# Optimization experiments

Measured on AMD Instinct MI355X. Metric: run time of the kernel, lower is better.

## Reference

```python
import jax, jax.numpy as jnp
import numpy as np

EPS = 1e-7
INF = 1e8
SOFT_CENTER_RADIUS = 3.0
TOPK = 13
IOU_WEIGHT = 3.0
NUM_CLASSES = 80
N_PRIORS = 33600
NUM_GT = 256
IMG = 1024.0


def setup_inputs() -> dict:
    key = jax.random.key(0)
    k1, k2, k3, k4, k5, k6, k7 = jax.random.split(key, 7)
    n, g, c = N_PRIORS, NUM_GT, NUM_CLASSES
    pred_scores = jax.random.normal(k1, (n, c), jnp.float32)
    # priors: (cx, cy, stride, stride)
    ctr = jax.random.uniform(k2, (n, 2), jnp.float32) * IMG
    stride = jnp.full((n, 1), 8.0, jnp.float32)
    priors = jnp.concatenate([ctr, stride, stride], axis=-1)
    # predicted boxes, x1y1x2y2
    pwh = jax.random.uniform(k3, (n, 2), jnp.float32) * 96.0 + 8.0
    pctr = jax.random.uniform(k4, (n, 2), jnp.float32) * IMG
    pred_bboxes = jnp.concatenate([pctr - pwh / 2, pctr + pwh / 2], axis=-1)
    # gt boxes, x1y1x2y2
    gwh = jax.random.uniform(k5, (g, 2), jnp.float32) * 192.0 + 16.0
    gctr = jax.random.uniform(k6, (g, 2), jnp.float32) * IMG
    gt_bboxes = jnp.concatenate([gctr - gwh / 2, gctr + gwh / 2], axis=-1)
    gt_labels = jax.random.randint(k7, (g,), 0, c, dtype=jnp.int32).astype(jnp.int64)
    return {"pred_scores": pred_scores, "priors": priors,
            "pred_bboxes": pred_bboxes, "gt_bboxes": gt_bboxes,
            "gt_labels": gt_labels}


def _pairwise_iou(a, b):
    # a: (n,4), b: (g,4), x1y1x2y2 -> (n,g)
    area_a = (a[:, 2] - a[:, 0]) * (a[:, 3] - a[:, 1])
    area_b = (b[:, 2] - b[:, 0]) * (b[:, 3] - b[:, 1])
    lt = jnp.maximum(a[:, None, :2], b[None, :, :2])
    rb = jnp.minimum(a[:, None, 2:], b[None, :, 2:])
    wh = jnp.clip(rb - lt, 0.0, None)
    inter = wh[..., 0] * wh[..., 1]
    union = area_a[:, None] + area_b[None, :] - inter
    return inter / jnp.maximum(union, 1e-6)


def reference(pred_scores, priors, pred_bboxes, gt_bboxes, gt_labels):
    n, g = pred_bboxes.shape[0], gt_bboxes.shape[0]
    gt_labels = gt_labels.astype(jnp.int32)

    # ---- find_inside_points (box_dim == 4) ----
    pts = priors[:, :2]                                   # (n,2)
    lt = pts[:, None, :] - gt_bboxes[None, :, :2]
    rb = gt_bboxes[None, :, 2:] - pts[:, None, :]
    is_in_gts = jnp.min(jnp.concatenate([lt, rb], -1), -1) > 0   # (n,g)
    pad_bbox_flag = gt_bboxes.sum(-1) > 0                        # (g,)
    is_in_gts = is_in_gts & pad_bbox_flag[None, :]
    valid_mask = jnp.any(is_in_gts, -1)                          # (n,)

    # ---- soft center prior ----
    gt_center = (gt_bboxes[:, :2] + gt_bboxes[:, 2:]) * 0.5      # (g,2)
    dist = jnp.sqrt(((pts[:, None, :] - gt_center[None, :, :]) ** 2).sum(-1))
    dist = dist / priors[:, 2:3]                                 # / stride
    dist = dist * valid_mask[:, None].astype(dist.dtype)
    soft_center_prior = jnp.power(10.0, dist - SOFT_CENTER_RADIUS)

    # ---- iou cost ----
    ious = _pairwise_iou(pred_bboxes, gt_bboxes)                 # (n,g)
    iou_cost = -jnp.log(ious + EPS) * IOU_WEIGHT

    # ---- soft classification cost (BCE-with-logits, iou targets) ----
    logits = pred_scores[:, gt_labels]                           # (n,g)
    scale = jnp.abs(ious - jax.nn.sigmoid(logits)) ** 2
    bce = jnp.maximum(logits, 0) - logits * ious + jnp.log1p(jnp.exp(-jnp.abs(logits)))
    cost = bce * scale + iou_cost + soft_center_prior
    cost = jnp.where(valid_mask[:, None], cost, INF)

    # ---- dynamic k matching (vectorized over GTs) ----
    K = min(TOPK, n)
    topk_ious, _ = jax.lax.top_k(ious.T, K)                      # (g,K)
    dynamic_ks = jnp.clip(topk_ious.sum(-1).astype(jnp.int32), 1, None)  # (g,)
    _, cand_idx = jax.lax.top_k(-cost.T, K)                      # (g,K) lowest-cost priors per gt
    sel = (jnp.arange(K)[None, :] < dynamic_ks[:, None]).astype(jnp.float32)
    matching = jnp.zeros((g, n), jnp.float32).at[
        jnp.arange(g)[:, None], cand_idx].set(sel).T             # (n,g)

    # resolve priors matched to multiple gts -> keep min-cost gt
    multi = matching.sum(-1) > 1
    onehot_min = jax.nn.one_hot(jnp.argmin(cost, -1), g, dtype=jnp.float32)
    matching = jnp.where(multi[:, None], onehot_min, matching)

    fg = matching.sum(-1) > 0
    matched_gt_inds = jnp.argmax(matching, -1)                   # (n,)
    matched_pred_ious = (matching * ious).sum(-1)                # (n,)

    final = fg & valid_mask
    assigned_gt_inds = jnp.where(final, matched_gt_inds + 1, 0)
    assigned_labels = jnp.where(final, gt_labels[matched_gt_inds], -1)
    max_overlaps = jnp.where(final, matched_pred_ious, -INF)
    return assigned_gt_inds, max_overlaps, assigned_labels
```

## Files before the change

### kernel.cpp

```cpp
#include <hip/hip_runtime.h>
#include <cstdint>

#define NPRI 33600
#define NGT  256
#define NCLS 80
#define KTOP 13
#define INF_F 1.0e8f
#define EPS_F 1e-7f
#define L10 3.3219280948873623f
#define SLC  4
#define SLEN (NPRI / SLC)
#define SCN_T 512
#define NW8 (SCN_T / 64)
#define CAPI 1536
#define CAPC 512
#define RFIX 5.5f
#define PREP_BLKS ((NPRI + 255) / 256)
#define NEGINF __int_as_float(0xff800000)

typedef unsigned long long u64;

__device__ __forceinline__ int get_label(const void* p, int j, int is64) {
    if (is64) return (int)((const long long*)p)[j];
    return ((const int*)p)[j];
}

__device__ __forceinline__ float wave_max_bc_f32(float v) {
    #pragma unroll
    for (int off = 32; off > 0; off >>= 1) v = fmaxf(v, __shfl_down(v, off, 64));
    return __int_as_float(__builtin_amdgcn_readfirstlane(__float_as_int(v)));
}
__device__ __forceinline__ u64 wave_min_bc_u64(u64 v) {
    #pragma unroll
    for (int off = 32; off > 0; off >>= 1) { u64 o = __shfl_down(v, off, 64); v = (o < v) ? o : v; }
    unsigned lo = (unsigned)__builtin_amdgcn_readfirstlane((int)(v & 0xffffffffull));
    unsigned hi = (unsigned)__builtin_amdgcn_readfirstlane((int)(v >> 32));
    return (((u64)hi) << 32) | lo;
}
template<int NSL>
__device__ __forceinline__ void wave_merge_max13_f32(float (&l)[NSL], float* dst, int lane) {
    int p = 0;
    for (int r = 0; r < KTOP; ++r) {
        float cur = NEGINF;
        #pragma unroll
        for (int s = 0; s < NSL; ++s) if (s == p) cur = l[NSL - 1 - s];
        float bm = wave_max_bc_f32(cur);
        u64 m = __ballot(cur == bm && bm != NEGINF);
        int first = __ffsll(m) - 1;
        if (lane == first) p++;
        if (lane == 0) dst[r] = bm;
    }
}
template<int NSL>
__device__ __forceinline__ void wave_merge_minN(u64 (&l)[NSL], u64* dst, int lane) {
    int p = 0;
    for (int r = 0; r < KTOP; ++r) {
        u64 cur = ~0ull;
        #pragma unroll
        for (int s = 0; s < NSL; ++s) if (s == p) cur = l[s];
        u64 bm = wave_min_bc_u64(cur);
        if (cur == bm && bm != ~0ull) p++;
        if (lane == 0) dst[r] = bm;
    }
}

__device__ __forceinline__ float iou_exact(float4 pb, float areap, float gx1, float gy1,
                                           float gx2, float gy2, float areag) {
    float iw = fmaxf(fminf(pb.z, gx2) - fmaxf(pb.x, gx1), 0.0f);
    float ih = fmaxf(fminf(pb.w, gy2) - fmaxf(pb.y, gy1), 0.0f);
    float inter = iw * ih;
    return inter / fmaxf(areap + areag - inter, 1e-6f);
}
__device__ __forceinline__ float cost_exact(float4 p2, float gcx, float gcy,
                                            float l, float iou) {
    float dx = p2.x - gcx, dy = p2.y - gcy;
    float dist = sqrtf(dx * dx + dy * dy) / p2.z;
    float soft = exp2f((dist - 3.0f) * L10);
    float sig = 1.0f / (1.0f + expf(-l));
    float dd = iou - sig;
    float bce = fmaxf(l, 0.0f) - l * iou + log1pf(expf(-fabsf(l)));
    float iouc = -logf(iou + EPS_F) * 3.0f;
    return bce * (dd * dd) + iouc + soft;
}

__global__ __launch_bounds__(256) void k_prep(
        const float* __restrict__ priors, const float* __restrict__ gt,
        const void* labels, const float* __restrict__ pboxes,
        float4* __restrict__ pbp,
        int* count, int* firstgt, int* flag, int* nmulti) {
    __shared__ float4 gbox[NGT];
    __shared__ int    gpad[NGT];
    __shared__ int    bad;
    const int tid = threadIdx.x;
    const int b = blockIdx.x;
    if (b == 0 && tid == 0) { bad = 0; *nmulti = 0; }
    {
        float4 bx = ((const float4*)gt)[tid];
        gbox[tid] = bx;
        gpad[tid] = ((bx.x + bx.y + bx.z + bx.w) > 0.0f) ? 1 : 0;
    }
    __syncthreads();
    if (b == 0 && tid < 128) {
        long long v = ((const long long*)labels)[tid];
        if (v < 0 || v >= NCLS) atomicOr(&bad, 1);
    }
    int i = b * 256 + tid;
    if (i < NPRI) {
        count[i] = 0; firstgt[i] = NGT;
        float4 pr = ((const float4*)priors)[i];
        float px = pr.x, py = pr.y;
        int v = 0;
        for (int j = 0; j < NGT; ++j) {
            float4 bx = gbox[j];
            float m = fminf(fminf(px - bx.x, py - bx.y), fminf(bx.z - px, bx.w - py));
            if (m > 0.0f && gpad[j]) { v = 1; break; }
        }
        pbp[2 * i]     = ((const float4*)pboxes)[i];
        pbp[2 * i + 1] = make_float4(px, py, pr.z, v ? 1.0f : 0.0f);
    }
    if (b == 0) {
        __syncthreads();
        if (tid == 0) *flag = bad ? 0 : 1;
    }
}

__global__ __launch_bounds__(SCN_T) void k_scan(
        const float* __restrict__ scores,
        const float4* __restrict__ pbp,
        const float* __restrict__ gt, const void* labels, const int* flag,
        float* __restrict__ part_iou, u64* __restrict__ part_cost) {
    const int tid = threadIdx.x, lane = tid & 63, wid = tid >> 6;
    const int j = blockIdx.x, slice = blockIdx.y;
    const int base = slice * SLEN;
    const int is64 = *flag;

    const float4 gb = ((const float4*)gt)[j];
    const float gx1 = gb.x, gy1 = gb.y, gx2 = gb.z, gy2 = gb.w;
    const float areag = (gx2 - gx1) * (gy2 - gy1);
    const float gcx = (gx1 + gx2) * 0.5f, gcy = (gy1 + gy2) * 0.5f;
    const int lab = get_label(labels, j, is64);

    __shared__ int s_ni, s_nc, s_mode;
    __shared__ float s_dmax;
    __shared__ float liou[CAPI];
    __shared__ int lcost[CAPC];
    __shared__ float wiof[NW8 * KTOP];
    __shared__ u64 wco[NW8 * KTOP];
    __shared__ u64 csel[KTOP];
    __shared__ u64 s_tauk;
    if (tid == 0) { s_ni = 0; s_nc = 0; }
    __syncthreads();

    for (int i = base + tid; i < base + SLEN; i += SCN_T) {
        float4 pb = pbp[2 * i];
        float4 p2 = pbp[2 * i + 1];
        float areap = (pb.z - pb.x) * (pb.w - pb.y);
        float iw = fmaxf(fminf(pb.z, gx2) - fmaxf(pb.x, gx1), 0.0f);
        float ih = fmaxf(fminf(pb.w, gy2) - fmaxf(pb.y, gy1), 0.0f);
        float inter = iw * ih;
        float iou = inter / fmaxf(areap + areag - inter, 1e-6f);
        if (iou > 0.0f) {
            int p = atomicAdd(&s_ni, 1);
            if (p < CAPI) liou[p] = iou;
        }
        if (p2.w != 0.0f) {
            float dx = p2.x - gcx, dy = p2.y - gcy;
            float rad = p2.z * RFIX;
            if (dx * dx + dy * dy <= rad * rad * (1.0f + 1e-5f)) {
                int p = atomicAdd(&s_nc, 1);
                if (p < CAPC) lcost[p] = i;
            }
        }
    }
    __syncthreads();
    const int ni = s_ni, nc = s_nc;
    const int ncc = (nc < CAPC) ? nc : CAPC;
    const bool fI = (ni > CAPI);

    const bool part = (tid < ncc);
    int ci = 0; float4 cpb, cp2; float lv = 0.0f;
    if (part) {
        ci = lcost[tid];
        cpb = pbp[2 * ci];
        cp2 = pbp[2 * ci + 1];
        lv = scores[(size_t)ci * NCLS + lab];
    }

    if (!fI) {
        float l3[3] = {NEGINF, NEGINF, NEGINF};
        for (int k = tid; k < ni; k += SCN_T) {
            float v = liou[k];
            if (v > l3[0]) {
                l3[0] = v;
                if (l3[0] > l3[1]) { float t = l3[0]; l3[0] = l3[1]; l3[1] = t; }
                if (l3[1] > l3[2]) { float t = l3[1]; l3[1] = l3[2]; l3[2] = t; }
            }
        }
        wave_merge_max13_f32<3>(l3, &wiof[wid * KTOP], lane);
    } else {
        float lf[KTOP];
        #pragma unroll
        for (int s = 0; s < KTOP; ++s) lf[s] = NEGINF;
        for (int i = base + tid; i < base + SLEN; i += SCN_T) {
            float4 pb = pbp[2 * i];
            float areap = (pb.z - pb.x) * (pb.w - pb.y);
            float iou = iou_exact(pb, areap, gx1, gy1, gx2, gy2, areag);
            if (iou > lf[0]) {
                lf[0] = iou;
                #pragma unroll
                for (int s = 0; s < KTOP - 1; ++s)
                    if (lf[s] > lf[s + 1]) { float t = lf[s]; lf[s] = lf[s + 1]; lf[s + 1] = t; }
            }
        }
        wave_merge_max13_f32<KTOP>(lf, &wiof[wid * KTOP], lane);
    }

    {
        u64 ck[1] = {~0ull};
        if (part) {
            float areap = (cpb.z - cpb.x) * (cpb.w - cpb.y);
            float iou = iou_exact(cpb, areap, gx1, gy1, gx2, gy2, areag);
            float ec = cost_exact(cp2, gcx, gcy, lv, iou);
            ck[0] = (((u64)__float_as_uint(ec)) << 32) | (unsigned)ci;
        }
        wave_merge_minN<1>(ck, &wco[wid * KTOP], lane);
    }
    __syncthreads();

    if (wid == 0) {
        float* dpi = part_iou + ((size_t)j * SLC + slice) * KTOP;
        int p = 0;
        for (int r = 0; r < KTOP; ++r) {
            float cur = (lane < NW8 && p < KTOP) ? wiof[lane * KTOP + p] : NEGINF;
            float bm = wave_max_bc_f32(cur);
            u64 m = __ballot(cur == bm && bm != NEGINF);
            int first = __ffsll(m) - 1;
            if (lane == first) p++;
            if (lane == 0) dpi[r] = bm;
        }
    } else if (wid == 1) {
        int p = 0;
        for (int r = 0; r < KTOP; ++r) {
            u64 cur = (lane < NW8 && p < KTOP) ? wco[lane * KTOP + p] : ~0ull;
            u64 bm = wave_min_bc_u64(cur);
            if (cur == bm && bm != ~0ull) p++;
            if (lane == 0) { csel[r] = bm; if (r == KTOP - 1) s_tauk = bm; }
        }
    }
    __syncthreads();
    if (tid == 0) {
        u64 tk = s_tauk;
        int mode; float dmax = 0.0f;
        if (tk == ~0ull) mode = 2;
        else {
            float tau = __uint_as_float((unsigned)(tk >> 32));
            if (!(tau < 9.0e7f)) mode = 2;
            else {
                dmax = 3.0f + __log2f(tau + 1e-5f) * (1.0f / L10) + 4e-3f;
                mode = (dmax > RFIX || nc > CAPC) ? 1 : 0;
            }
        }
        s_mode = mode; s_dmax = dmax;
    }
    __syncthreads();
    int mode = s_mode;

    if (mode == 1) {
        const float dmax = s_dmax;
        if (tid == 0) s_nc = 0;
        __syncthreads();
        for (int i = base + tid; i < base + SLEN; i += SCN_T) {
            float4 p2 = pbp[2 * i + 1];
            if (p2.w != 0.0f) {
                float dx = p2.x - gcx, dy = p2.y - gcy;
                float rad = p2.z * dmax;
                if (dx * dx + dy * dy <= rad * rad * (1.0f + 1e-5f)) {
                    int p = atomicAdd(&s_nc, 1);
                    if (p < CAPC) lcost[p] = i;
                }
            }
        }
        __syncthreads();
        int nc2 = s_nc;
        if (nc2 > CAPC) {
            mode = 2;
        } else {
            u64 ck[1] = {~0ull};
            if (tid < nc2) {
                int i = lcost[tid];
                float4 pb = pbp[2 * i];
                float4 p2 = pbp[2 * i + 1];
                float areap = (pb.z - pb.x) * (pb.w - pb.y);
                float iou = iou_exact(pb, areap, gx1, gy1, gx2, gy2, areag);
                float ec = cost_exact(p2, gcx, gcy, scores[(size_t)i * NCLS + lab], iou);
                ck[0] = (((u64)__float_as_uint(ec)) << 32) | (unsigned)i;
            }
            wave_merge_minN<1>(ck, &wco[wid * KTOP], lane);
            __syncthreads();
            if (wid == 0) {
                int p = 0;
                for (int r = 0; r < KTOP; ++r) {
                    u64 cur = (lane < NW8 && p < KTOP) ? wco[lane * KTOP + p] : ~0ull;
                    u64 bm = wave_min_bc_u64(cur);
                    if (cur == bm && bm != ~0ull) p++;
                    if (lane == 0) csel[r] = bm;
                }
            }
            __syncthreads();
        }
    }
    if (mode == 2) {
        u64 lf[KTOP];
        #pragma unroll
        for (int s = 0; s < KTOP; ++s) lf[s] = ~0ull;
        for (int i = base + tid; i < base + SLEN; i += SCN_T) {
            float4 pb = pbp[2 * i];
            float4 p2 = pbp[2 * i + 1];
            float areap = (pb.z - pb.x) * (pb.w - pb.y);
            float iou = iou_exact(pb, areap, gx1, gy1, gx2, gy2, areag);
            float ec = INF_F;
            if (p2.w != 0.0f) ec = cost_exact(p2, gcx, gcy, scores[(size_t)i * NCLS + lab], iou);
            u64 k2 = (((u64)__float_as_uint(ec)) << 32) | (unsigned)i;
            if (k2 < lf[KTOP - 1]) {
                lf[KTOP - 1] = k2;
                #pragma unroll
                for (int s = KTOP - 1; s > 0; --s)
                    if (lf[s] < lf[s - 1]) { u64 t = lf[s]; lf[s] = lf[s - 1]; lf[s - 1] = t; }
            }
        }
        wave_merge_minN<KTOP>(lf, &wco[wid * KTOP], lane);
        __syncthreads();
        if (wid == 0) {
            int p = 0;
            for (int r = 0; r < KTOP; ++r) {
                u64 cur = (lane < NW8 && p < KTOP) ? wco[lane * KTOP + p] : ~0ull;
                u64 bm = wave_min_bc_u64(cur);
                if (cur == bm && bm != ~0ull) p++;
                if (lane == 0) csel[r] = bm;
            }
        }
        __syncthreads();
    }
    if (tid < KTOP) {
        u64* dpc = part_cost + ((size_t)j * SLC + slice) * KTOP;
        dpc[tid] = csel[tid];
    }
}

__global__ __launch_bounds__(64) void k_merge(
        const float* __restrict__ part_iou, const u64* __restrict__ part_cost,
        int* count, int* firstgt) {
    const int j = blockIdx.x;
    const int lane = threadIdx.x;
    float vi = (lane < SLC * KTOP) ? part_iou[(size_t)j * SLC * KTOP + lane] : NEGINF;
    float tsum = 0.0f;
    for (int r = 0; r < KTOP; ++r) {
        float bm = wave_max_bc_f32(vi);
        u64 m = __ballot(vi == bm && bm != NEGINF);
        int first = __ffsll(m) - 1;
        if (lane == first) vi = NEGINF;
        tsum += (bm == NEGINF) ? 0.0f : bm;
    }
    int ks = (int)tsum;
    if (ks < 1) ks = 1;
    u64 kc = (lane < SLC * KTOP) ? part_cost[(size_t)j * SLC * KTOP + lane] : ~0ull;
    u64 mine = ~0ull;
    for (int r = 0; r < KTOP; ++r) {
        u64 bm = wave_min_bc_u64(kc);
        if (kc == bm && bm != ~0ull) kc = ~0ull;
        if (lane == r) mine = bm;
    }
    if (lane < KTOP && lane < ks && mine != ~0ull) {
        int idx = (int)(unsigned)(mine & 0xFFFFFFFFull);
        atomicAdd(&count[idx], 1);
        atomicMin(&firstgt[idx], j);
    }
}

__global__ __launch_bounds__(256) void k_assign(
        const float4* __restrict__ pbp, const float* __restrict__ gt,
        const void* labels, const int* flag,
        const int* __restrict__ count, const int* __restrict__ firstgt,
        int* nmulti, int* mlist, float* __restrict__ out) {
    __shared__ float4 gbox[NGT];
    __shared__ int glab[NGT];
    __shared__ float gareas[NGT];
    int tid = threadIdx.x;
    int is64 = *flag;
    {
        float4 b = ((const float4*)gt)[tid];
        gbox[tid] = b;
        glab[tid] = get_label(labels, tid, is64);
        gareas[tid] = (b.z - b.x) * (b.w - b.y);
    }
    __syncthreads();
    int i = blockIdx.x * 256 + tid;
    if (i >= NPRI) return;
    float4 p2 = pbp[2 * i + 1];
    int v = (p2.w != 0.0f) ? 1 : 0;
    int c = count[i];
    float o0 = 0.0f, o1 = -INF_F, o2 = -1.0f;
    if (v && c == 1) {
        int j = firstgt[i];
        float4 pb = pbp[2 * i];
        float areap = (pb.z - pb.x) * (pb.w - pb.y);
        float4 g = gbox[j];
        float iw = fmaxf(fminf(pb.z, g.z) - fmaxf(pb.x, g.x), 0.0f);
        float ih = fmaxf(fminf(pb.w, g.w) - fmaxf(pb.y, g.y), 0.0f);
        float inter = iw * ih;
        float iou = inter / fmaxf(areap + gareas[j] - inter, 1e-6f);
        o0 = (float)(j + 1); o1 = iou; o2 = (float)glab[j];
    } else if (v && c > 1) {
        int pos = atomicAdd(nmulti, 1);
        mlist[pos] = i;
    }
    out[i] = o0;
    out[NPRI + i] = o1;
    out[2 * NPRI + i] = o2;
}

__global__ __launch_bounds__(256) void k_multi(
        const float* __restrict__ scores,
        const float4* __restrict__ pbp, const float* __restrict__ gt,
        const void* labels, const int* flag,
        const int* __restrict__ nmulti, const int* __restrict__ mlist,
        float* __restrict__ out) {
    __shared__ float4 gbox[NGT];
    __shared__ int glab[NGT];
    __shared__ float gcxs[NGT], gcys[NGT], gareas[NGT];
    __shared__ u64 red4[4];
    const int tid = threadIdx.x;
    const int is64 = *flag;
    {
        float4 b = ((const float4*)gt)[tid];
        gbox[tid] = b;
        glab[tid] = get_label(labels, tid, is64);
        gcxs[tid] = (b.x + b.z) * 0.5f;
        gcys[tid] = (b.y + b.w) * 0.5f;
        gareas[tid] = (b.z - b.x) * (b.w - b.y);
    }
    __syncthreads();
    const int nm = *nmulti;
    const int j = tid;
    for (int m = blockIdx.x; m < nm; m += gridDim.x) {
        const int i = mlist[m];
        float4 pb = pbp[2 * i];
        float4 p2 = pbp[2 * i + 1];
        float areap = (pb.z - pb.x) * (pb.w - pb.y);

        float4 g = gbox[j];
        float iw = fmaxf(fminf(pb.z, g.z) - fmaxf(pb.x, g.x), 0.0f);
        float ih = fmaxf(fminf(pb.w, g.w) - fmaxf(pb.y, g.y), 0.0f);
        float inter = iw * ih;
        float iou = inter / fmaxf(areap + gareas[j] - inter, 1e-6f);
        float dx = p2.x - gcxs[j], dy = p2.y - gcys[j];
        float dist = sqrtf(dx * dx + dy * dy) / p2.z;
        float soft = exp2f((dist - 3.0f) * L10);
        float l = scores[(size_t)i * NCLS + glab[j]];
        float sig = 1.0f / (1.0f + expf(-l));
        float dd = iou - sig;
        float bce = fmaxf(l, 0.0f) - l * iou + log1pf(expf(-fabsf(l)));
        float cost = bce * (dd * dd) + (-logf(iou + EPS_F) * 3.0f) + soft;

        u64 key = (((u64)__float_as_uint(cost)) << 32) | (unsigned)j;
        u64 v = key;
        #pragma unroll
        for (int off = 32; off > 0; off >>= 1) {
            u64 o = __shfl_down(v, off, 64);
            v = (o < v) ? o : v;
        }
        if ((tid & 63) == 0) red4[tid >> 6] = v;
        __syncthreads();
        u64 best = red4[0];
        #pragma unroll
        for (int q = 1; q < 4; ++q) best = (red4[q] < best) ? red4[q] : best;
        if (key == best) {
            out[i] = (float)(j + 1);
            out[NPRI + i] = iou;
            out[2 * NPRI + i] = (float)glab[j];
        }
        __syncthreads();
    }
}

extern "C" void kernel_launch(void* const* d_in, const int* in_sizes, int n_in,
                              void* d_out, int out_size, void* d_ws, size_t ws_size,
                              hipStream_t stream) {
    const float* scores = (const float*)d_in[0];
    const float* priors = (const float*)d_in[1];
    const float* pboxes = (const float*)d_in[2];
    const float* gt     = (const float*)d_in[3];
    const void*  labels = d_in[4];
    float* out = (float*)d_out;

    char* ws = (char*)d_ws;
    size_t off = 0;
    auto alloc = [&](size_t bytes) { size_t o = off; off = (off + bytes + 255) & ~(size_t)255; return o; };
    int*    flag     = (int*)(ws + alloc(4));
    int*    nmulti   = (int*)(ws + alloc(4));
    int*    count    = (int*)(ws + alloc((size_t)NPRI * 4));
    int*    firstgt  = (int*)(ws + alloc((size_t)NPRI * 4));
    int*    mlist    = (int*)(ws + alloc((size_t)NPRI * 4));
    float*  part_iou = (float*)(ws + alloc((size_t)NGT * SLC * KTOP * 4));
    u64*    part_cost= (u64*)(ws + alloc((size_t)NGT * SLC * KTOP * 8));
    float4* pbp      = (float4*)(ws + alloc((size_t)NPRI * 32));
    (void)ws_size;

    hipLaunchKernelGGL(k_prep, dim3(PREP_BLKS), dim3(256), 0, stream,
                       priors, gt, labels, pboxes, pbp, count, firstgt, flag, nmulti);
    hipLaunchKernelGGL(k_scan, dim3(NGT, SLC), dim3(SCN_T), 0, stream,
                       scores, pbp, gt, labels, flag, part_iou, part_cost);
    hipLaunchKernelGGL(k_merge, dim3(NGT), dim3(64), 0, stream,
                       part_iou, part_cost, count, firstgt);
    hipLaunchKernelGGL(k_assign, dim3((NPRI + 255) / 256), dim3(256), 0, stream,
                       pbp, gt, labels, flag, count, firstgt, nmulti, mlist, out);
    hipLaunchKernelGGL(k_multi, dim3(256), dim3(256), 0, stream,
                       scores, pbp, gt, labels, flag, nmulti, mlist, out);
}
```

Measured before the change: 164.2 us.

## Aggregate LDS atomics per wave and split cost/IoU top-k across single waves

The candidate-compaction loop now uses wave ballots with one LDS atomicAdd per wave instead of per-lane atomics. The per-thread candidate cost evaluation and cross-wave merge are replaced by a single wave computing the top-13 cost over all compacted candidates while a second wave concurrently computes the IoU top-13 directly into the output. This removes several block barriers and shared-memory merge rounds, at the cost of serialising candidate work onto one wave, with a 13-entry sorted list per lane.

Measured after the change: 160.2 us. -2.5%, faster.

```diff
diff --git a/kernel.cpp b/kernel.cpp
--- a/kernel.cpp
+++ b/kernel.cpp
@@ -12,6 +12,7 @@
 #define SLEN (NPRI / SLC)
 #define SCN_T 512
 #define NW8 (SCN_T / 64)
+#define NIT  ((SLEN + SCN_T - 1) / SCN_T)
 #define CAPI 1536
 #define CAPC 512
 #define RFIX 5.5f
@@ -147,27 +148,50 @@
     __shared__ float wiof[NW8 * KTOP];
     __shared__ u64 wco[NW8 * KTOP];
     __shared__ u64 csel[KTOP];
-    __shared__ u64 s_tauk;
     if (tid == 0) { s_ni = 0; s_nc = 0; }
     __syncthreads();
 
-    for (int i = base + tid; i < base + SLEN; i += SCN_T) {
-        float4 pb = pbp[2 * i];
-        float4 p2 = pbp[2 * i + 1];
-        float areap = (pb.z - pb.x) * (pb.w - pb.y);
-        float iw = fmaxf(fminf(pb.z, gx2) - fmaxf(pb.x, gx1), 0.0f);
-        float ih = fmaxf(fminf(pb.w, gy2) - fmaxf(pb.y, gy1), 0.0f);
-        float inter = iw * ih;
-        float iou = inter / fmaxf(areap + areag - inter, 1e-6f);
-        if (iou > 0.0f) {
-            int p = atomicAdd(&s_ni, 1);
-            if (p < CAPI) liou[p] = iou;
-        }
-        if (p2.w != 0.0f) {
-            float dx = p2.x - gcx, dy = p2.y - gcy;
-            float rad = p2.z * RFIX;
-            if (dx * dx + dy * dy <= rad * rad * (1.0f + 1e-5f)) {
-                int p = atomicAdd(&s_nc, 1);
+    for (int it = 0; it < NIT; ++it) {
+        int i = base + tid + it * SCN_T;
+        bool inb = (i < base + SLEN);
+        float iou = 0.0f;
+        bool pc = false;
+        if (inb) {
+            float4 pb = pbp[2 * i];
+            float4 p2 = pbp[2 * i + 1];
+            float areap = (pb.z - pb.x) * (pb.w - pb.y);
+            float iw = fmaxf(fminf(pb.z, gx2) - fmaxf(pb.x, gx1), 0.0f);
+            float ih = fmaxf(fminf(pb.w, gy2) - fmaxf(pb.y, gy1), 0.0f);
+            float inter = iw * ih;
+            iou = inter / fmaxf(areap + areag - inter, 1e-6f);
+            if (p2.w != 0.0f) {
+                float dx = p2.x - gcx, dy = p2.y - gcy;
+                float rad = p2.z * RFIX;
+                pc = (dx * dx + dy * dy <= rad * rad * (1.0f + 1e-5f));
+            }
+        }
+        bool pi = inb && (iou > 0.0f);
+        u64 mi = __ballot(pi);
+        if (mi) {
+            int lead = __ffsll(mi) - 1;
+            int cnt = __popcll(mi);
+            int bs = 0;
+            if (lane == lead) bs = atomicAdd(&s_ni, cnt);
+            bs = __shfl(bs, lead, 64);
+            if (pi) {
+                int p = bs + __popcll(mi & ((1ull << lane) - 1ull));
+                if (p < CAPI) liou[p] = iou;
+            }
+        }
+        u64 mc = __ballot(pc);
+        if (mc) {
+            int lead = __ffsll(mc) - 1;
+            int cnt = __popcll(mc);
+            int bs = 0;
+            if (lane == lead) bs = atomicAdd(&s_nc, cnt);
+            bs = __shfl(bs, lead, 64);
+            if (pc) {
+                int p = bs + __popcll(mc & ((1ull << lane) - 1ull));
                 if (p < CAPC) lcost[p] = i;
             }
         }
@@ -177,27 +201,59 @@
     const int ncc = (nc < CAPC) ? nc : CAPC;
     const bool fI = (ni > CAPI);
 
-    const bool part = (tid < ncc);
-    int ci = 0; float4 cpb, cp2; float lv = 0.0f;
-    if (part) {
-        ci = lcost[tid];
-        cpb = pbp[2 * ci];
-        cp2 = pbp[2 * ci + 1];
-        lv = scores[(size_t)ci * NCLS + lab];
-    }
-
-    if (!fI) {
-        float l3[3] = {NEGINF, NEGINF, NEGINF};
-        for (int k = tid; k < ni; k += SCN_T) {
+    if (wid == 0) {
+        u64 lf[KTOP];
+        #pragma unroll
+        for (int s = 0; s < KTOP; ++s) lf[s] = ~0ull;
+        for (int k = lane; k < ncc; k += 64) {
+            int i = lcost[k];
+            float4 pb = pbp[2 * i];
+            float4 p2 = pbp[2 * i + 1];
+            float areap = (pb.z - pb.x) * (pb.w - pb.y);
+            float iou = iou_exact(pb, areap, gx1, gy1, gx2, gy2, areag);
+            float ec = cost_exact(p2, gcx, gcy, scores[(size_t)i * NCLS + lab], iou);
+            u64 ck = (((u64)__float_as_uint(ec)) << 32) | (unsigned)i;
+            if (ck < lf[KTOP - 1]) {
+                lf[KTOP - 1] = ck;
+                #pragma unroll
+                for (int s = KTOP - 1; s > 0; --s)
+                    if (lf[s] < lf[s - 1]) { u64 t = lf[s]; lf[s] = lf[s - 1]; lf[s - 1] = t; }
+            }
+        }
+        wave_merge_minN<KTOP>(lf, csel, lane);
+        if (lane == 0) {
+            u64 tk = csel[KTOP - 1];
+            int mode; float dmax = 0.0f;
+            if (tk == ~0ull) mode = 2;
+            else {
+                float tau = __uint_as_float((unsigned)(tk >> 32));
+                if (!(tau < 9.0e7f)) mode = 2;
+                else {
+                    dmax = 3.0f + __log2f(tau + 1e-5f) * (1.0f / L10) + 4e-3f;
+                    mode = (dmax > RFIX || nc > CAPC) ? 1 : 0;
+                }
+            }
+            s_mode = mode; s_dmax = dmax;
+        }
+    } else if (wid == 1 && !fI) {
+        float lf[KTOP];
+        #pragma unroll
+        for (int s = 0; s < KTOP; ++s) lf[s] = NEGINF;
+        int nn = (ni < CAPI) ? ni : CAPI;
+        for (int k = lane; k < nn; k += 64) {
             float v = liou[k];
-            if (v > l3[0]) {
-                l3[0] = v;
-                if (l3[0] > l3[1]) { float t = l3[0]; l3[0] = l3[1]; l3[1] = t; }
-                if (l3[1] > l3[2]) { float t = l3[1]; l3[1] = l3[2]; l3[2] = t; }
-            }
-        }
-        wave_merge_max13_f32<3>(l3, &wiof[wid * KTOP], lane);
-    } else {
+            if (v > lf[0]) {
+                lf[0] = v;
+                #pragma unroll
+                for (int s = 0; s < KTOP - 1; ++s)
+                    if (lf[s] > lf[s + 1]) { float t = lf[s]; lf[s] = lf[s + 1]; lf[s + 1] = t; }
+            }
+        }
+        wave_merge_max13_f32<KTOP>(lf, part_iou + ((size_t)j * SLC + slice) * KTOP, lane);
+    }
+    __syncthreads();
+
+    if (fI) {
         float lf[KTOP];
         #pragma unroll
         for (int s = 0; s < KTOP; ++s) lf[s] = NEGINF;
@@ -213,58 +269,23 @@
             }
         }
         wave_merge_max13_f32<KTOP>(lf, &wiof[wid * KTOP], lane);
-    }
-
-    {
-        u64 ck[1] = {~0ull};
-        if (part) {
-            float areap = (cpb.z - cpb.x) * (cpb.w - cpb.y);
-            float iou = iou_exact(cpb, areap, gx1, gy1, gx2, gy2, areag);
-            float ec = cost_exact(cp2, gcx, gcy, lv, iou);
-            ck[0] = (((u64)__float_as_uint(ec)) << 32) | (unsigned)ci;
-        }
-        wave_merge_minN<1>(ck, &wco[wid * KTOP], lane);
-    }
-    __syncthreads();
-
-    if (wid == 0) {
-        float* dpi = part_iou + ((size_t)j * SLC + slice) * KTOP;
-        int p = 0;
-        for (int r = 0; r < KTOP; ++r) {
-            float cur = (lane < NW8 && p < KTOP) ? wiof[lane * KTOP + p] : NEGINF;
-            float bm = wave_max_bc_f32(cur);
-            u64 m = __ballot(cur == bm && bm != NEGINF);
-            int first = __ffsll(m) - 1;
-            if (lane == first) p++;
-            if (lane == 0) dpi[r] = bm;
-        }
-    } else if (wid == 1) {
-        int p = 0;
-        for (int r = 0; r < KTOP; ++r) {
-            u64 cur = (lane < NW8 && p < KTOP) ? wco[lane * KTOP + p] : ~0ull;
-            u64 bm = wave_min_bc_u64(cur);
-            if (cur == bm && bm != ~0ull) p++;
-            if (lane == 0) { csel[r] = bm; if (r == KTOP - 1) s_tauk = bm; }
-        }
-    }
-    __syncthreads();
-    if (tid == 0) {
-        u64 tk = s_tauk;
-        int mode; float dmax = 0.0f;
-        if (tk == ~0ull) mode = 2;
-        else {
-            float tau = __uint_as_float((unsigned)(tk >> 32));
-            if (!(tau < 9.0e7f)) mode = 2;
-            else {
-                dmax = 3.0f + __log2f(tau + 1e-5f) * (1.0f / L10) + 4e-3f;
-                mode = (dmax > RFIX || nc > CAPC) ? 1 : 0;
-            }
-        }
-        s_mode = mode; s_dmax = dmax;
-    }
-    __syncthreads();
+        __syncthreads();
+        if (wid == 0) {
+            float* dpi = part_iou + ((size_t)j * SLC + slice) * KTOP;
+            int p = 0;
+            for (int r = 0; r < KTOP; ++r) {
+                float cur = (lane < NW8 && p < KTOP) ? wiof[lane * KTOP + p] : NEGINF;
+                float bm = wave_max_bc_f32(cur);
+                u64 m = __ballot(cur == bm && bm != NEGINF);
+                int first = __ffsll(m) - 1;
+                if (lane == first) p++;
+                if (lane == 0) dpi[r] = bm;
+            }
+        }
+        __syncthreads();
+    }
+
     int mode = s_mode;
-
     if (mode == 1) {
         const float dmax = s_dmax;
         if (tid == 0) s_nc = 0;
@@ -282,32 +303,32 @@
         }
         __syncthreads();
         int nc2 = s_nc;
-        if (nc2 > CAPC) {
+        if (nc2 <= CAPC) {
+            if (wid == 0) {
+                u64 lf[KTOP];
+                #pragma unroll
+                for (int s = 0; s < KTOP; ++s) lf[s] = ~0ull;
+                for (int k = lane; k < nc2; k += 64) {
+                    int i = lcost[k];
+                    float4 pb = pbp[2 * i];
+                    float4 p2 = pbp[2 * i + 1];
+                    float areap = (pb.z - pb.x) * (pb.w - pb.y);
+                    float iou = iou_exact(pb, areap, gx1, gy1, gx2, gy2, areag);
+                    float ec = cost_exact(p2, gcx, gcy, scores[(size_t)i * NCLS + lab], iou);
+                    u64 ck = (((u64)__float_as_uint(ec)) << 32) | (unsigned)i;
+                    if (ck < lf[KTOP - 1]) {
+                        lf[KTOP - 1] = ck;
+                        #pragma unroll
+                        for (int s = KTOP - 1; s > 0; --s)
+                            if (lf[s] < lf[s - 1]) { u64 t = lf[s]; lf[s] = lf[s - 1]; lf[s - 1] = t; }
+                    }
+                }
+                wave_merge_minN<KTOP>(lf, csel, lane);
+            }
+        } else {
             mode = 2;
-        } else {
-            u64 ck[1] = {~0ull};
-            if (tid < nc2) {
-                int i = lcost[tid];
-                float4 pb = pbp[2 * i];
-                float4 p2 = pbp[2 * i + 1];
-                float areap = (pb.z - pb.x) * (pb.w - pb.y);
-                float iou = iou_exact(pb, areap, gx1, gy1, gx2, gy2, areag);
-                float ec = cost_exact(p2, gcx, gcy, scores[(size_t)i * NCLS + lab], iou);
-                ck[0] = (((u64)__float_as_uint(ec)) << 32) | (unsigned)i;
-            }
-            wave_merge_minN<1>(ck, &wco[wid * KTOP], lane);
-            __syncthreads();
-            if (wid == 0) {
-                int p = 0;
-                for (int r = 0; r < KTOP; ++r) {
-                    u64 cur = (lane < NW8 && p < KTOP) ? wco[lane * KTOP + p] : ~0ull;
-                    u64 bm = wave_min_bc_u64(cur);
-                    if (cur == bm && bm != ~0ull) p++;
-                    if (lane == 0) csel[r] = bm;
-                }
-            }
-            __syncthreads();
-        }
+        }
+        __syncthreads();
     }
     if (mode == 2) {
         u64 lf[KTOP];
```
